# Performance work log

Measured on AMD Instinct MI355X. Metric: run time of the kernel, lower is better.

Reference implementation:

```python
import jax, jax.numpy as jnp
import numpy as np

B, L, C, Y, DIM = 64, 64, 4, 0, 2  # batch, lattice size, n_colors, tau-shift, shift axis


def _coloring_probes():
    # k x k block coloring for C colors (C must be a perfect square here; C=4 -> k=2)
    k = int(round(np.sqrt(C)))
    i = np.arange(L)[:, None]
    j = np.arange(L)[None, :]
    col = (i % k) * k + (j % k)  # (L, L) color index per site
    probes = (col[None, :, :] == np.arange(C)[:, None, None]).astype(np.float32)
    return jnp.asarray(probes)  # (C, L, L) one-hot color masks


def _gelu(x):
    return jax.nn.gelu(x, approximate=False)  # torch nn.GELU default = exact erf


def _forward(x, sW1, sb1, sW2, sb2, sW3, sb3, aW1, ab1, aW2, ab2):
    # site features: phi, 2D lattice laplacian (periodic), phi_{x+tau}, phi_{x-tau}
    lap = (jnp.roll(x, 1, 1) + jnp.roll(x, -1, 1)
           + jnp.roll(x, 1, 2) + jnp.roll(x, -1, 2) - 4.0 * x)
    phi_tau = jnp.roll(x, -Y, axis=DIM)
    phi_mtau = jnp.roll(x, Y, axis=DIM)
    f = jnp.stack([x, lap, phi_tau, phi_mtau], axis=-1)  # (B, L, L, 4)
    h = _gelu(f @ sW1 + sb1)
    h = _gelu(h @ sW2 + sb2)
    h = (h @ sW3 + sb3)[..., 0]                          # (B, L, L)
    h_mean = h.mean(axis=(1, 2))
    h_var = jnp.var(h, axis=(1, 2), ddof=1)              # torch .var() is unbiased
    h_sq_mean = (h * h).mean(axis=(1, 2))
    a = jnp.stack([h_mean, h_var, h_sq_mean], axis=1)    # (B, 3)
    a = _gelu(a @ aW1 + ab1)
    return (a @ aW2 + ab2)[..., 0]                       # (B,)


def setup_inputs() -> dict:
    key = jax.random.key(0)
    ks = jax.random.split(key, 8)

    def w(k, shape, fan_in):
        return jax.random.normal(k, shape, jnp.float32) / np.sqrt(fan_in).astype(np.float32)

    return {
        "x": jax.random.normal(ks[0], (B, L, L), jnp.float32),
        "signs": jax.random.randint(ks[1], (C, B, L, L), 0, 2, jnp.int32),
        "site_W1": w(ks[2], (4, 128), 4),
        "site_b1": jnp.zeros((128,), jnp.float32),
        "site_W2": w(ks[3], (128, 128), 128),
        "site_b2": jnp.zeros((128,), jnp.float32),
        "site_W3": w(ks[4], (128, 1), 128),
        "site_b3": jnp.zeros((1,), jnp.float32),
        "agg_W1": w(ks[5], (3, 64), 3),
        "agg_b1": jnp.zeros((64,), jnp.float32),
        "agg_W2": w(ks[6], (64, 1), 64),
        "agg_b2": jnp.zeros((1,), jnp.float32),
    }


def reference(x, signs, site_W1, site_b1, site_W2, site_b2, site_W3, site_b3,
              agg_W1, agg_b1, agg_W2, agg_b2):
    params = (site_W1, site_b1, site_W2, site_b2, site_W3, site_b3,
              agg_W1, agg_b1, agg_W2, agg_b2)
    fsum = lambda xx: _forward(xx, *params).sum()  # batches are independent, so sum is safe

    # first-order gradient grad_x F, shape (B, L, L)
    grad = jax.grad(fsum)(x)

    # probing laplacian with coloring + Rademacher signs, batched over colors
    probes = _coloring_probes()                                   # (C, L, L)
    z = (2.0 * signs.astype(jnp.float32) - 1.0) * probes[:, None]  # (C, B, L, L)
    # hvp_c = H @ z_c via forward-over-reverse AD (replaces per-color autograd.grad loop)
    hvp = jax.vmap(lambda zc: jax.jvp(jax.grad(fsum), (x,), (zc,))[1])(z)  # (C, B, L, L)
    lapl = jnp.sum(hvp * z, axis=(0, 2, 3))                       # (B,)

    # pack (grad, lapl) into one array: (B, L*L + 1)
    return jnp.concatenate([grad.reshape(B, -1), lapl[:, None]], axis=1)
```

## Files before the change

### kernel.cpp

```cpp
#include <hip/hip_runtime.h>
#include <hip/hip_bf16.h>
#include <math.h>

typedef unsigned short ushort_t;
typedef unsigned int   u32;
typedef __attribute__((ext_vector_type(8))) short s8v;
typedef __attribute__((ext_vector_type(4))) float f4v;
typedef __attribute__((ext_vector_type(2))) float f2v;

#define LL 64
#define NB 64
#define NSITE 4096
#define BN 262144
#define RED_OFF 0
#define WA_OFF  11264
#define WB_OFF  11392
#define PL_OFF  12288
#define BF_OFF  (PL_OFF + 6*BN)

#if __has_builtin(__builtin_amdgcn_exp2f)
#define EXP2F(x) __builtin_amdgcn_exp2f(x)
#else
#define EXP2F(x) __expf(0.6931471805599453f*(x))
#endif

__device__ __forceinline__ void gelu3(float u, float &h, float &d, float &e){
  float E   = __expf(-0.5f * u * u);
  float phi = 0.3989422804014327f * E;
  float az  = fabsf(u) * 0.70710678118654752f;
  float t   = __builtin_amdgcn_rcpf(1.0f + 0.3275911f * az);
  float p   = t*(0.254829592f + t*(-0.284496736f + t*(1.421413741f + t*(-1.453152027f + t*1.061405429f))));
  float erfabs = 1.0f - p * E;
  float erfv   = __builtin_copysignf(erfabs, u);
  float Phi = 0.5f * (1.0f + erfv);
  h = u * Phi;
  d = Phi + u * phi;
  e = phi * (2.0f - u * u);
}

__device__ __forceinline__ void gelu3x2(f2v u, f2v &h, f2v &d, f2v &e){
  f2v u2 = u * u;
  f2v m  = u2 * (-0.72134752044448170368f);
  f2v E;  E.x = EXP2F(m.x); E.y = EXP2F(m.y);
  f2v phi = 0.3989422804014327f * E;
  f2v az;
  az.x = fabsf(u.x) * 0.70710678118654752f;
  az.y = fabsf(u.y) * 0.70710678118654752f;
  f2v den = 0.3275911f * az + 1.0f;
  f2v t;  t.x = __builtin_amdgcn_rcpf(den.x); t.y = __builtin_amdgcn_rcpf(den.y);
  f2v p = t*(0.254829592f + t*(-0.284496736f + t*(1.421413741f + t*(-1.453152027f + t*1.061405429f))));
  f2v erfabs = 1.0f - p * E;
  f2v erfv;
  erfv.x = __builtin_copysignf(erfabs.x, u.x);
  erfv.y = __builtin_copysignf(erfabs.y, u.y);
  f2v Phi = 0.5f * erfv + 0.5f;
  h = u * Phi;
  d = u * phi + Phi;
  e = phi * (2.0f - u2);
}

#define DPP_ADD(v, ctrl) { \
  int _si = __builtin_amdgcn_update_dpp(0, __builtin_bit_cast(int, v), ctrl, 0xf, 0xf, true); \
  v += __builtin_bit_cast(float, _si); }

__device__ __forceinline__ float redjb16(float v){
  DPP_ADD(v, 0xB1);
  DPP_ADD(v, 0x4E);
  DPP_ADD(v, 0x124);
  DPP_ADD(v, 0x128);
  return v;
}
__device__ __forceinline__ float red64(float v){
  v = redjb16(v);
  v += __shfl_xor(v, 16);
  v += __shfl_xor(v, 32);
  return v;
}

__device__ __forceinline__ ushort_t bf16rne(float v){
  union { float f; u32 i; } x; x.f = v;
  u32 r = x.i + 0x7FFFu + ((x.i >> 16) & 1u);
  return (ushort_t)(r >> 16);
}
__device__ __forceinline__ u32 pkbf(float a, float b){
  __hip_bfloat162 t = __float22bfloat162_rn(make_float2(a, b));
  u32 r;
  __builtin_memcpy(&r, &t, sizeof(r));
  return r;
}
__device__ __forceinline__ u32 pkbf2(f2v v){
  return pkbf(v.x, v.y);
}

__global__ __launch_bounds__(256, 4) void k_pre(
    const float* __restrict__ W1g, const float* __restrict__ W2g,
    float* __restrict__ ws, float* __restrict__ out)
{
  int t = blockIdx.x * 256 + threadIdx.x;
  if (blockIdx.x == 0 && threadIdx.x < 128) {
    int k = threadIdx.x;
    ws[WA_OFF + k] = W1g[k] + W1g[256+k] + W1g[384+k];
    ws[WB_OFF + k] = W1g[128+k];
  }
  if (blockIdx.x == 1 && threadIdx.x < 64) {
    out[(size_t)threadIdx.x*4097 + 4096] = 0.f;
  }
  short* BF = (short*)(ws + BF_OFF);
  int w = t >> 9, nt = (t >> 8) & 1, kt = (t >> 6) & 3, lane = t & 63;
  int q = lane >> 4, nlo = lane & 15;
  int n = w*32 + nt*16 + nlo;
  s8v vh;
  #pragma unroll
  for (int jj = 0; jj < 8; ++jj) {
    int k = kt*32 + q*8 + jj;
    vh[jj] = (short)bf16rne(W2g[k*128 + n]);
  }
  *(s8v*)&BF[t*8] = vh;
}

__global__ __launch_bounds__(256, 4) void k_c1(
    const float* __restrict__ xg, const int* __restrict__ signs,
    const float* __restrict__ b1g, const float* __restrict__ b2g,
    const float* __restrict__ W3g, const float* __restrict__ b3g,
    float* __restrict__ ws)
{
  __shared__ alignas(16) short AF[12288];
  __shared__ float xS[6][64];
  __shared__ char  zS[6][64];
  __shared__ float EP[16][7][4];

  const int tid  = threadIdx.x;
  const int lane = tid & 63;
  const int w    = tid >> 6;
  const int rg4  = (lane >> 4) << 2;

  const int blk = blockIdx.x;
  const int b   = blk >> 4;
  const int i0  = (blk & 15) << 2;

  const s8v* BhT = (const s8v*)((const short*)(ws + BF_OFF)) + (w*512 + lane);

  float4 b2H[2], w3H[2];
  #pragma unroll
  for (int nt = 0; nt < 2; ++nt) {
    int n0 = w*32 + nt*16 + rg4;
    b2H[nt] = *(const float4*)(b2g + n0);
    w3H[nt] = *(const float4*)(W3g + n0);
  }
  float b3v = b3g[0];

  const int s_  = tid & 15;
  const int ko_ = tid >> 4;
  float4 waH[2], wbH[2], b1H[2];
  #pragma unroll
  for (int half = 0; half < 2; ++half) {
    int k0 = ko_*8 + half*4;
    waH[half] = *(const float4*)(ws + WA_OFF + k0);
    wbH[half] = *(const float4*)(ws + WB_OFF + k0);
    b1H[half] = *(const float4*)(b1g + k0);
  }

  for (int t = tid; t < 384; t += 256) {
    int r = t >> 6, j = t & 63;
    int gr = (i0 - 1 + r) & 63;
    xS[r][j] = xg[(size_t)b*NSITE + gr*64 + j];
    int c = ((gr & 1) << 1) | (j & 1);
    zS[r][j] = (char)(2*signs[((c*NB + b)*LL + gr)*LL + j] - 1);
  }
  __syncthreads();

  float racc[10];
  #pragma unroll
  for (int n = 0; n < 10; ++n) racc[n] = 0.f;

  const f4v Zf = {0.f, 0.f, 0.f, 0.f};

  #pragma unroll 1
  for (int ch = 0; ch < 16; ++ch) {
    const int lr = 1 + (ch >> 2);
    const int jb = ch & 3;
    const int i  = i0 + (ch >> 2);

    s8v pb00 = BhT[0],  pb10 = BhT[256];
    s8v pb01 = BhT[64], pb11 = BhT[320];

    {
      int j = jb*16 + s_, jm = (j+63)&63, jp = (j+1)&63;
      float p = xS[lr][j];
      float l = xS[lr-1][j] + xS[lr+1][j] + xS[lr][jm] + xS[lr][jp] - 4.0f*p;
      u32 vv[6][4];
      #pragma unroll
      for (int half = 0; half < 2; ++half) {
        const float* waA = (const float*)&waH[half];
        const float* wbA = (const float*)&wbH[half];
        const float* b1A = (const float*)&b1H[half];
        #pragma unroll
        for (int pr = 0; pr < 2; ++pr) {
          f2v wa = {waA[pr*2], waA[pr*2+1]};
          f2v wb = {wbA[pr*2], wbA[pr*2+1]};
          f2v bb = {b1A[pr*2], b1A[pr*2+1]};
          f2v u = p*wa + l*wb + bb;
          f2v h, dd, ee;
          gelu3x2(u, h, dd, ee);
          int c = half*2 + pr;
          vv[0][c] = pkbf2(h);
          vv[1][c] = pkbf2(dd*wa);
          vv[2][c] = pkbf2(dd*wb);
          f2v ea = ee*wa, eb = ee*wb;
          vv[3][c] = pkbf2(ea*wa);
          vv[4][c] = pkbf2(ea*wb);
          vv[5][c] = pkbf2(eb*wb);
        }
      }
      short* base = &AF[(ko_>>2)*3072 + ((ko_&3)*16 + s_)*8];
      #pragma unroll
      for (int pp = 0; pp < 6; ++pp)
        *(int4*)&base[pp*512] = make_int4((int)vv[pp][0], (int)vv[pp][1],
                                          (int)vv[pp][2], (int)vv[pp][3]);
    }
    __syncthreads();

    f4v acc[6][2];
    __builtin_amdgcn_s_setprio(1);
    {
      const short* base = &AF[lane*8];
      #pragma unroll
      for (int pp = 0; pp < 6; ++pp) {
        s8v ah = *(const s8v*)&base[pp*512];
        acc[pp][0] = __builtin_amdgcn_mfma_f32_16x16x32_bf16(pb00, ah, Zf, 0, 0, 0);
        acc[pp][1] = __builtin_amdgcn_mfma_f32_16x16x32_bf16(pb10, ah, Zf, 0, 0, 0);
      }
    }
    s8v bh0 = pb01, bh1 = pb11;
    #pragma unroll 1
    for (int kt = 1; kt < 4; ++kt) {
      s8v nh0 = bh0, nh1 = bh1;
      if (kt != 3) {
        int o = (kt + 1) * 64;
        nh0 = BhT[o]; nh1 = BhT[256 + o];
      }
      const short* base = &AF[kt*3072 + lane*8];
      #pragma unroll
      for (int pp = 0; pp < 6; ++pp) {
        s8v ah = *(const s8v*)&base[pp*512];
        acc[pp][0] = __builtin_amdgcn_mfma_f32_16x16x32_bf16(bh0, ah, acc[pp][0], 0, 0, 0);
        acc[pp][1] = __builtin_amdgcn_mfma_f32_16x16x32_bf16(bh1, ah, acc[pp][1], 0, 0, 0);
      }
      bh0 = nh0; bh1 = nh1;
    }
    __builtin_amdgcn_s_setprio(0);

    {
      f2v qh = {0.f,0.f}, qA = {0.f,0.f}, qB = {0.f,0.f};
      f2v qa = {0.f,0.f}, qb = {0.f,0.f}, qc = {0.f,0.f};
      #pragma unroll
      for (int nt = 0; nt < 2; ++nt) {
        const float* b2A = (const float*)&b2H[nt];
        const float* w3A = (const float*)&w3H[nt];
        #pragma unroll
        for (int pr = 0; pr < 2; ++pr) {
          const int r0 = pr*2;
          f2v uu  = (f2v){acc[0][nt][r0], acc[0][nt][r0+1]}
                  + (f2v){b2A[r0], b2A[r0+1]};
          f2v w3p = {w3A[r0], w3A[r0+1]};
          f2v h2, d2, e2;
          gelu3x2(uu, h2, d2, e2);
          f2v wd = w3p*d2, we = w3p*e2;
          f2v A  = {acc[1][nt][r0], acc[1][nt][r0+1]};
          f2v Bv = {acc[2][nt][r0], acc[2][nt][r0+1]};
          f2v t3 = {acc[3][nt][r0], acc[3][nt][r0+1]};
          f2v t4 = {acc[4][nt][r0], acc[4][nt][r0+1]};
          f2v t5 = {acc[5][nt][r0], acc[5][nt][r0+1]};
          qh += w3p*h2;
          qA += wd*A;
          qB += wd*Bv;
          qa += we*(A*A)   + wd*t3;
          qb += we*(A*Bv)  + wd*t4;
          qc += we*(Bv*Bv) + wd*t5;
        }
      }
      float sh = qh.x + qh.y;
      float sA = qA.x + qA.y;
      float sB = qB.x + qB.y;
      float sa = qa.x + qa.y;
      float sb = qb.x + qb.y;
      float sc = qc.x + qc.y;
      sh += __shfl_xor(sh, 16); sh += __shfl_xor(sh, 32);
      sA += __shfl_xor(sA, 16); sA += __shfl_xor(sA, 32);
      sB += __shfl_xor(sB, 16); sB += __shfl_xor(sB, 32);
      sa += __shfl_xor(sa, 16); sa += __shfl_xor(sa, 32);
      sb += __shfl_xor(sb, 16); sb += __shfl_xor(sb, 32);
      sc += __shfl_xor(sc, 16); sc += __shfl_xor(sc, 32);
      if (lane < 16) {
        EP[lane][0][w] = sh;
        EP[lane][1][w] = sA;
        EP[lane][2][w] = sB;
        EP[lane][3][w] = sa;
        EP[lane][4][w] = sb;
        EP[lane][5][w] = sc;
      }
    }
    __syncthreads();

    if (tid < 16) {
      int s = tid;
      float h = 0.f, RA = 0.f, RB = 0.f, TAa = 0.f, TAb = 0.f, TBb = 0.f;
      #pragma unroll
      for (int ww = 0; ww < 4; ++ww) {
        h   += EP[s][0][ww];
        RA  += EP[s][1][ww];
        RB  += EP[s][2][ww];
        TAa += EP[s][3][ww];
        TAb += EP[s][4][ww];
        TBb += EP[s][5][ww];
      }
      h += b3v;
      float* P = ws + PL_OFF;
      int j = jb*16 + s;
      size_t site = (size_t)b*NSITE + i*64 + j;
      P[0*BN + site] = h;
      P[1*BN + site] = RA;
      P[2*BN + site] = RB;
      P[3*BN + site] = TAa;
      P[4*BN + site] = TAb;
      P[5*BN + site] = TBb;

      int jm = (j+63)&63, jp = (j+1)&63;
      int c0 = ((i & 1) << 1) | (j & 1);
      float hd[4] = {0.f, 0.f, 0.f, 0.f};
      hd[c0]     = (float)zS[lr][j] * (RA - 4.0f*RB);
      hd[c0 ^ 1] = (float)(zS[lr][jm] + zS[lr][jp]) * RB;
      hd[c0 ^ 2] = (float)(zS[lr-1][j] + zS[lr+1][j]) * RB;
      racc[0] += h;
      racc[1] += h*h;
      #pragma unroll
      for (int cc = 0; cc < 4; ++cc) {
        racc[2+cc] += hd[cc];
        racc[6+cc] += h*hd[cc];
      }
    }
  }

  if (tid < 16) {
    #pragma unroll
    for (int n = 0; n < 10; ++n) racc[n] = redjb16(racc[n]);
    if (tid == 0) {
      #pragma unroll
      for (int n = 0; n < 10; ++n) ws[RED_OFF + blk*10 + n] = racc[n];
    }
  }
}

__global__ __launch_bounds__(256, 4) void k_c2(
    const int* __restrict__ signs,
    const float* __restrict__ aW1g, const float* __restrict__ ab1g,
    const float* __restrict__ aW2g,
    float* __restrict__ ws, float* __restrict__ out)
{
  __shared__ float part[4];
  __shared__ float coefL[10];
  __shared__ float redS[10];
  __shared__ float cbS[6][64];
  int blk = blockIdx.x;
  int b = blk >> 4, rg = blk & 15;
  int tid = threadIdx.x;

  if (tid < 160) {
    int qq = tid >> 4, g = tid & 15;
    float v = ws[RED_OFF + (b*16 + g)*10 + qq];
    v = redjb16(v);
    if (g == 0) redS[qq] = v;
  }
  __syncthreads();

  if (tid < 64) {
    int k = tid;
    const float Nf = 4096.0f, Nm1 = 4095.0f;
    float S1 = redS[0], S2 = redS[1];
    float m = S1/Nf, q = S2/Nf;
    float v = (S2 - S1*S1/Nf)/Nm1;
    float w0 = aW1g[k], w1 = aW1g[64+k], w2 = aW1g[128+k];
    float t = m*w0 + v*w1 + q*w2 + ab1g[k];
    float gh, gd, ge;
    gelu3(t, gh, gd, ge);
    float o = aW2g[k];
    float g1o = gd*o, g2o = ge*o;
    float da0 = w0*g1o, da1 = w1*g1o, da2 = w2*g1o;
    float M00 = w0*w0*g2o, M01 = w0*w1*g2o, M02 = w0*w2*g2o;
    float M11 = w1*w1*g2o, M12 = w1*w2*g2o, M22 = w2*w2*g2o;
    da0 = red64(da0); da1 = red64(da1); da2 = red64(da2);
    M00 = red64(M00); M01 = red64(M01); M02 = red64(M02);
    M11 = red64(M11); M12 = red64(M12); M22 = red64(M22);
    if (k == 0) {
      coefL[0] = da0/Nf - 2.0f*da1*m/Nm1;
      coefL[1] = 2.0f*da1/Nm1 + 2.0f*da2/Nf;
      #pragma unroll
      for (int c = 0; c < 4; ++c) {
        float s1 = redS[2 + c], s2 = redS[6 + c];
        float md = s1/Nf, qd = 2.0f*s2/Nf;
        float vd = (2.0f*s2 - 2.0f*S1*s1/Nf)/Nm1;
        float dd0 = M00*md + M01*vd + M02*qd;
        float dd1 = M01*md + M11*vd + M12*qd;
        float dd2 = M02*md + M12*vd + M22*qd;
        coefL[2+c] = dd0/Nf - 2.0f*(dd1*m + da1*md)/Nm1;
        coefL[6+c] = 2.0f*dd1/Nm1 + 2.0f*dd2/Nf;
      }
    }
  }
  __syncthreads();

  const float* P = ws + PL_OFF;
  int base = b*NSITE;
  float alpha = coefL[0], beta = coefL[1];

  for (int t = tid; t < 384; t += 256) {
    int r = t >> 6, jj = t & 63;
    int gr = (rg*4 - 1 + r) & 63;
    int sidx = base + gr*64 + jj;
    cbS[r][jj] = (alpha + beta*P[sidx]) * P[2*BN + sidx];
  }
  __syncthreads();

  int rl = tid >> 6, j = tid & 63;
  int i = rg*4 + rl;
  int im=(i+63)&63, ip=(i+1)&63, jm=(j+63)&63, jp=(j+1)&63;
  int s  = base + i*64 + j;
  float h  = P[s], RA = P[BN+s], RB = P[2*BN+s];
  float TAa= P[3*BN+s], TAb = P[4*BN+s], TBb = P[5*BN+s];
  float g  = alpha + beta*h;
  int lr2 = rl + 1;
  float cb  = cbS[lr2][j];
  float cbu = cbS[lr2-1][j], cbd = cbS[lr2+1][j];
  float cbl = cbS[lr2][jm],  cbr = cbS[lr2][jp];
  float grad = g*RA + (cbu + cbd + cbl + cbr - 4.0f*cb);
  out[(size_t)b*4097 + i*64 + j] = grad;

  int c0 = ((i & 1) << 1) | (j & 1);
  int c1 = c0 ^ 1, c2 = c0 ^ 2;
  float zv = 2.0f*(float)signs[((c0*NB + b)*LL + i )*LL + j ] - 1.0f;
  float zl = 2.0f*(float)signs[((c1*NB + b)*LL + i )*LL + jm] - 1.0f;
  float zr = 2.0f*(float)signs[((c1*NB + b)*LL + i )*LL + jp] - 1.0f;
  float zu = 2.0f*(float)signs[((c2*NB + b)*LL + im)*LL + j ] - 1.0f;
  float zd = 2.0f*(float)signs[((c2*NB + b)*LL + ip)*LL + j ] - 1.0f;
  float sjr = zl + zr, sud = zu + zd;
  float hd0 = zv*(RA - 4.0f*RB);
  float hd1 = sjr*RB, hd2 = sud*RB;
  float gd0 = coefL[2+c0] + coefL[6+c0]*h + beta*hd0;
  float gd1 = coefL[2+c1] + coefL[6+c1]*h + beta*hd1;
  float gd2 = coefL[2+c2] + coefL[6+c2]*h + beta*hd2;
  float ca0 = gd0*RA + g*( zv*TAa - 4.0f*zv*TAb );
  float cb0 = gd0*RB + g*( zv*TAb - 4.0f*zv*TBb );
  float cb1 = gd1*RB + g*( sjr*TBb );
  float cb2 = gd2*RB + g*( sud*TBb );
  float contrib = zv*ca0 - 4.0f*zv*cb0 + sjr*cb1 + sud*cb2;

  float vsum = red64(contrib);
  int wv = tid >> 6;
  if ((tid & 63) == 0) part[wv] = vsum;
  __syncthreads();
  if (tid == 0)
    atomicAdd(out + (size_t)b*4097 + 4096,
              part[0] + part[1] + part[2] + part[3]);
}

extern "C" void kernel_launch(void* const* d_in, const int* in_sizes, int n_in,
                              void* d_out, int out_size, void* d_ws, size_t ws_size,
                              hipStream_t stream) {
  const float* xg    = (const float*)d_in[0];
  const int*   signs = (const int*)d_in[1];
  const float* W1    = (const float*)d_in[2];
  const float* b1    = (const float*)d_in[3];
  const float* W2    = (const float*)d_in[4];
  const float* b2    = (const float*)d_in[5];
  const float* W3    = (const float*)d_in[6];
  const float* b3    = (const float*)d_in[7];
  const float* aW1   = (const float*)d_in[8];
  const float* ab1   = (const float*)d_in[9];
  const float* aW2   = (const float*)d_in[10];
  float* ws  = (float*)d_ws;
  float* out = (float*)d_out;

  hipLaunchKernelGGL(k_pre, dim3(8),    dim3(256), 0, stream, W1, W2, ws, out);
  hipLaunchKernelGGL(k_c1,  dim3(1024), dim3(256), 0, stream,
                     xg, signs, b1, b2, W3, b3, ws);
  hipLaunchKernelGGL(k_c2,  dim3(1024), dim3(256), 0, stream,
                     signs, aW1, ab1, aW2, ws, out);
}
```

Before: 190.7 us.

## Double-buffer A fragments and epilogue partials to cut per-chunk barriers

Double-buffers the LDS A-fragment tile and the epilogue partial-sum array so each chunk needs only one __syncthreads instead of two. The final per-site reduction for a chunk is deferred to the next iteration. Each wave first consumes its own k-slice before the barrier, and the remaining k-slices are visited in a rotated order per wave. The extra LDS raises occupancy pressure, so launch bounds drop from 4 to 3 blocks per CU.

```diff
diff --git a/kernel.cpp b/kernel.cpp
--- a/kernel.cpp
+++ b/kernel.cpp
@@ -118,16 +118,16 @@
   *(s8v*)&BF[t*8] = vh;
 }
 
-__global__ __launch_bounds__(256, 4) void k_c1(
+__global__ __launch_bounds__(256, 3) void k_c1(
     const float* __restrict__ xg, const int* __restrict__ signs,
     const float* __restrict__ b1g, const float* __restrict__ b2g,
     const float* __restrict__ W3g, const float* __restrict__ b3g,
     float* __restrict__ ws)
 {
-  __shared__ alignas(16) short AF[12288];
+  __shared__ alignas(16) short AF[2][12288];
   __shared__ float xS[6][64];
   __shared__ char  zS[6][64];
-  __shared__ float EP[16][7][4];
+  __shared__ float EP[2][16][6][4];
 
   const int tid  = threadIdx.x;
   const int lane = tid & 63;
@@ -139,6 +139,7 @@
   const int i0  = (blk & 15) << 2;
 
   const s8v* BhT = (const s8v*)((const short*)(ws + BF_OFF)) + (w*512 + lane);
+  const int ktA = (w + 1) & 3, ktB = (w + 2) & 3, ktC = (w + 3) & 3;
 
   float4 b2H[2], w3H[2];
   #pragma unroll
@@ -174,15 +175,16 @@
   for (int n = 0; n < 10; ++n) racc[n] = 0.f;
 
   const f4v Zf = {0.f, 0.f, 0.f, 0.f};
+  int lrP = 0, jbP = 0, iP = 0;
 
   #pragma unroll 1
   for (int ch = 0; ch < 16; ++ch) {
+    const int cur = ch & 1;
     const int lr = 1 + (ch >> 2);
     const int jb = ch & 3;
     const int i  = i0 + (ch >> 2);
 
-    s8v pb00 = BhT[0],  pb10 = BhT[256];
-    s8v pb01 = BhT[64], pb11 = BhT[320];
+    s8v pb0 = BhT[w*64], pb1 = BhT[256 + w*64];
 
     {
       int j = jb*16 + s_, jm = (j+63)&63, jp = (j+1)&63;
@@ -212,34 +214,31 @@
           vv[5][c] = pkbf2(eb*wb);
         }
       }
-      short* base = &AF[(ko_>>2)*3072 + ((ko_&3)*16 + s_)*8];
+      short* base = &AF[cur][(ko_>>2)*3072 + ((ko_&3)*16 + s_)*8];
       #pragma unroll
       for (int pp = 0; pp < 6; ++pp)
         *(int4*)&base[pp*512] = make_int4((int)vv[pp][0], (int)vv[pp][1],
                                           (int)vv[pp][2], (int)vv[pp][3]);
     }
+
+    f4v acc[6][2];
+    {
+      const short* base = &AF[cur][w*3072 + lane*8];
+      #pragma unroll
+      for (int pp = 0; pp < 6; ++pp) {
+        s8v ah = *(const s8v*)&base[pp*512];
+        acc[pp][0] = __builtin_amdgcn_mfma_f32_16x16x32_bf16(pb0, ah, Zf, 0, 0, 0);
+        acc[pp][1] = __builtin_amdgcn_mfma_f32_16x16x32_bf16(pb1, ah, Zf, 0, 0, 0);
+      }
+    }
+    s8v bh0 = BhT[ktA*64], bh1 = BhT[256 + ktA*64];
+
     __syncthreads();
 
-    f4v acc[6][2];
     __builtin_amdgcn_s_setprio(1);
     {
-      const short* base = &AF[lane*8];
-      #pragma unroll
-      for (int pp = 0; pp < 6; ++pp) {
-        s8v ah = *(const s8v*)&base[pp*512];
-        acc[pp][0] = __builtin_amdgcn_mfma_f32_16x16x32_bf16(pb00, ah, Zf, 0, 0, 0);
-        acc[pp][1] = __builtin_amdgcn_mfma_f32_16x16x32_bf16(pb10, ah, Zf, 0, 0, 0);
-      }
-    }
-    s8v bh0 = pb01, bh1 = pb11;
-    #pragma unroll 1
-    for (int kt = 1; kt < 4; ++kt) {
-      s8v nh0 = bh0, nh1 = bh1;
-      if (kt != 3) {
-        int o = (kt + 1) * 64;
-        nh0 = BhT[o]; nh1 = BhT[256 + o];
-      }
-      const short* base = &AF[kt*3072 + lane*8];
+      s8v nh0 = BhT[ktB*64], nh1 = BhT[256 + ktB*64];
+      const short* base = &AF[cur][ktA*3072 + lane*8];
       #pragma unroll
       for (int pp = 0; pp < 6; ++pp) {
         s8v ah = *(const s8v*)&base[pp*512];
@@ -247,6 +246,26 @@
         acc[pp][1] = __builtin_amdgcn_mfma_f32_16x16x32_bf16(bh1, ah, acc[pp][1], 0, 0, 0);
       }
       bh0 = nh0; bh1 = nh1;
+    }
+    {
+      s8v nh0 = BhT[ktC*64], nh1 = BhT[256 + ktC*64];
+      const short* base = &AF[cur][ktB*3072 + lane*8];
+      #pragma unroll
+      for (int pp = 0; pp < 6; ++pp) {
+        s8v ah = *(const s8v*)&base[pp*512];
+        acc[pp][0] = __builtin_amdgcn_mfma_f32_16x16x32_bf16(bh0, ah, acc[pp][0], 0, 0, 0);
+        acc[pp][1] = __builtin_amdgcn_mfma_f32_16x16x32_bf16(bh1, ah, acc[pp][1], 0, 0, 0);
+      }
+      bh0 = nh0; bh1 = nh1;
+    }
+    {
+      const short* base = &AF[cur][ktC*3072 + lane*8];
+      #pragma unroll
+      for (int pp = 0; pp < 6; ++pp) {
+        s8v ah = *(const s8v*)&base[pp*512];
+        acc[pp][0] = __builtin_amdgcn_mfma_f32_16x16x32_bf16(bh0, ah, acc[pp][0], 0, 0, 0);
+        acc[pp][1] = __builtin_amdgcn_mfma_f32_16x16x32_bf16(bh1, ah, acc[pp][1], 0, 0, 0);
+      }
     }
     __builtin_amdgcn_s_setprio(0);
 
@@ -292,32 +311,31 @@
       sb += __shfl_xor(sb, 16); sb += __shfl_xor(sb, 32);
       sc += __shfl_xor(sc, 16); sc += __shfl_xor(sc, 32);
       if (lane < 16) {
-        EP[lane][0][w] = sh;
-        EP[lane][1][w] = sA;
-        EP[lane][2][w] = sB;
-        EP[lane][3][w] = sa;
-        EP[lane][4][w] = sb;
-        EP[lane][5][w] = sc;
-      }
-    }
-    __syncthreads();
-
-    if (tid < 16) {
+        EP[cur][lane][0][w] = sh;
+        EP[cur][lane][1][w] = sA;
+        EP[cur][lane][2][w] = sB;
+        EP[cur][lane][3][w] = sa;
+        EP[cur][lane][4][w] = sb;
+        EP[cur][lane][5][w] = sc;
+      }
+    }
+
+    if (ch > 0 && tid < 16) {
       int s = tid;
       float h = 0.f, RA = 0.f, RB = 0.f, TAa = 0.f, TAb = 0.f, TBb = 0.f;
       #pragma unroll
       for (int ww = 0; ww < 4; ++ww) {
-        h   += EP[s][0][ww];
-        RA  += EP[s][1][ww];
-        RB  += EP[s][2][ww];
-        TAa += EP[s][3][ww];
-        TAb += EP[s][4][ww];
-        TBb += EP[s][5][ww];
+        h   += EP[cur^1][s][0][ww];
+        RA  += EP[cur^1][s][1][ww];
+        RB  += EP[cur^1][s][2][ww];
+        TAa += EP[cur^1][s][3][ww];
+        TAb += EP[cur^1][s][4][ww];
+        TBb += EP[cur^1][s][5][ww];
       }
       h += b3v;
       float* P = ws + PL_OFF;
-      int j = jb*16 + s;
-      size_t site = (size_t)b*NSITE + i*64 + j;
+      int j = jbP*16 + s;
+      size_t site = (size_t)b*NSITE + iP*64 + j;
       P[0*BN + site] = h;
       P[1*BN + site] = RA;
       P[2*BN + site] = RB;
@@ -326,11 +344,11 @@
       P[5*BN + site] = TBb;
 
       int jm = (j+63)&63, jp = (j+1)&63;
-      int c0 = ((i & 1) << 1) | (j & 1);
+      int c0 = ((iP & 1) << 1) | (j & 1);
       float hd[4] = {0.f, 0.f, 0.f, 0.f};
-      hd[c0]     = (float)zS[lr][j] * (RA - 4.0f*RB);
-      hd[c0 ^ 1] = (float)(zS[lr][jm] + zS[lr][jp]) * RB;
-      hd[c0 ^ 2] = (float)(zS[lr-1][j] + zS[lr+1][j]) * RB;
+      hd[c0]     = (float)zS[lrP][j] * (RA - 4.0f*RB);
+      hd[c0 ^ 1] = (float)(zS[lrP][jm] + zS[lrP][jp]) * RB;
+      hd[c0 ^ 2] = (float)(zS[lrP-1][j] + zS[lrP+1][j]) * RB;
       racc[0] += h;
       racc[1] += h*h;
       #pragma unroll
@@ -339,9 +357,49 @@
         racc[6+cc] += h*hd[cc];
       }
     }
-  }
+
+    lrP = lr; jbP = jb; iP = i;
+  }
+
+  __syncthreads();
 
   if (tid < 16) {
+    int s = tid;
+    float h = 0.f, RA = 0.f, RB = 0.f, TAa = 0.f, TAb = 0.f, TBb = 0.f;
+    #pragma unroll
+    for (int ww = 0; ww < 4; ++ww) {
+      h   += EP[1][s][0][ww];
+      RA  += EP[1][s][1][ww];
+      RB  += EP[1][s][2][ww];
+      TAa += EP[1][s][3][ww];
+      TAb += EP[1][s][4][ww];
+      TBb += EP[1][s][5][ww];
+    }
+    h += b3v;
+    float* P = ws + PL_OFF;
+    int j = jbP*16 + s;
+    size_t site = (size_t)b*NSITE + iP*64 + j;
+    P[0*BN + site] = h;
+    P[1*BN + site] = RA;
+    P[2*BN + site] = RB;
+    P[3*BN + site] = TAa;
+    P[4*BN + site] = TAb;
+    P[5*BN + site] = TBb;
+
+    int jm = (j+63)&63, jp = (j+1)&63;
+    int c0 = ((iP & 1) << 1) | (j & 1);
+    float hd[4] = {0.f, 0.f, 0.f, 0.f};
+    hd[c0]     = (float)zS[lrP][j] * (RA - 4.0f*RB);
+    hd[c0 ^ 1] = (float)(zS[lrP][jm] + zS[lrP][jp]) * RB;
+    hd[c0 ^ 2] = (float)(zS[lrP-1][j] + zS[lrP+1][j]) * RB;
+    racc[0] += h;
+    racc[1] += h*h;
+    #pragma unroll
+    for (int cc = 0; cc < 4; ++cc) {
+      racc[2+cc] += hd[cc];
+      racc[6+cc] += h*hd[cc];
+    }
+
     #pragma unroll
     for (int n = 0; n < 10; ++n) racc[n] = redjb16(racc[n]);
     if (tid == 0) {
```

New measurement: 188.6 us. About the same (-1.1%).
